# Kernel tuning notes

Measured on AMD Instinct MI355X. Metric: run time of the kernel, lower is better.

## Reference

```python
import jax, jax.numpy as jnp
import numpy as np

B, T, C, H = 8, 1024, 128, 8
BLOCK = 1024  # block_size; wpe has BLOCK+1 rows, last is padding (zeros)
E = C // H


def layer_norm(x, g, b, eps=1e-5):
    mu = jnp.mean(x, axis=-1, keepdims=True)
    var = jnp.var(x, axis=-1, keepdims=True)
    return (x - mu) * jax.lax.rsqrt(var + eps) * g + b


def setup_inputs() -> dict:
    key = jax.random.key(0)
    ks = jax.random.split(key, 7)
    x = jax.random.normal(ks[0], (B, T, C), dtype=jnp.float32)
    Wq = jax.random.normal(ks[1], (C, C), dtype=jnp.float32) * 0.02
    Wk = jax.random.normal(ks[2], (C, C), dtype=jnp.float32) * 0.02
    Wv = jax.random.normal(ks[3], (C, C), dtype=jnp.float32) * 0.02
    Wp = jax.random.normal(ks[4], (C, C), dtype=jnp.float32) * 0.02
    wpe = jax.random.normal(ks[5], (BLOCK + 1, C), dtype=jnp.float32) * 0.02
    wpe = wpe.at[BLOCK].set(0.0)  # padding_idx row is zero
    ln_g = jnp.ones((C,), dtype=jnp.float32)
    ln_b = jnp.zeros((C,), dtype=jnp.float32)
    return {"x": x, "Wq": Wq, "Wk": Wk, "Wv": Wv, "Wp": Wp,
            "wpe": wpe, "ln_g": ln_g, "ln_b": ln_b}


def reference(x, Wq, Wk, Wv, Wp, wpe, ln_g, ln_b):
    Bx, Tx, Cx = x.shape
    ln_x = layer_norm(x, ln_g, ln_b)
    # project and split heads: [B, H, T, E]
    q = (ln_x @ Wq).reshape(Bx, Tx, H, E).transpose(0, 2, 1, 3)
    k = (ln_x @ Wk).reshape(Bx, Tx, H, E).transpose(0, 2, 1, 3)
    v = (ln_x @ Wv).reshape(Bx, Tx, H, E).transpose(0, 2, 1, 3)
    # relative position indices: i-j, negatives -> padding row BLOCK
    i = jnp.arange(Tx)[:, None]
    j = jnp.arange(Tx)[None, :]
    rel_idx = jnp.where(i - j < 0, BLOCK, i - j)  # [T, T]
    rel = wpe[rel_idx].reshape(Tx, Tx, H, E)      # [T, T, H, E]
    scale = 1.0 / np.sqrt(E).astype(np.float32)
    scores = (jnp.einsum('bhte,bhse->bhts', q, k)
              + jnp.einsum('tshe,bhte->bhts', rel, q)) * scale
    causal = (j <= i)  # [T, T]
    scores = jnp.where(causal[None, None, :, :], scores, jnp.float32(-jnp.inf))
    attn = jax.nn.softmax(scores, axis=-1)
    y = jnp.einsum('bhts,bhse->bhte', attn, v)    # [B, H, T, E]
    y = y.transpose(0, 2, 1, 3).reshape(Bx, Tx, Cx)
    return y @ Wp + x
```

## Files before the change

### kernel.cpp

```cpp
#include <hip/hip_runtime.h>
#include <hip/hip_bf16.h>

#define B 8
#define T 1024
#define C 128
#define H 8
#define E 16
#define BH (B*H)

typedef __attribute__((ext_vector_type(4)))  short bf16x4;
typedef __attribute__((ext_vector_type(8)))  short bf16x8;
typedef __attribute__((ext_vector_type(16))) float f32x16;

#define QSCALE 0.36067376022224085f

__device__ __forceinline__ unsigned short bfbits(float x) {
    __hip_bfloat16 h = __float2bfloat16(x);
    return __builtin_bit_cast(unsigned short, h);
}
__device__ __forceinline__ unsigned pack2(float a, float b) {
    return (unsigned)bfbits(a) | ((unsigned)bfbits(b) << 16);
}
__device__ __forceinline__ unsigned packtr(float a, float b) {
    return (__builtin_bit_cast(unsigned, a) >> 16) | (__builtin_bit_cast(unsigned, b) & 0xffff0000u);
}

__global__ __launch_bounds__(C) void k_prep(
    const float* __restrict__ wpe,
    const float* __restrict__ Wq, const float* __restrict__ Wk,
    const float* __restrict__ Wv, const float* __restrict__ Wp,
    __hip_bfloat16* __restrict__ Wpb,
    __hip_bfloat16* __restrict__ WT,
    __hip_bfloat16* __restrict__ WpT)
{
    int bid = blockIdx.x, tid = threadIdx.x;
    if (bid < 1025) {
        int h = tid >> 4, e = tid & 15;
        Wpb[((size_t)h * 1025 + bid) * 16 + e] = __float2bfloat16(wpe[(size_t)bid * C + tid]);
    } else {
        int n = bid - 1025;
        if (n < 128)      WT[n * C + tid]          = __float2bfloat16(Wq[tid * C + n] * QSCALE);
        else if (n < 256) WT[n * C + tid]          = __float2bfloat16(Wk[tid * C + (n - 128)]);
        else if (n < 384) WT[n * C + tid]          = __float2bfloat16(Wv[tid * C + (n - 256)]);
        else              WpT[(n - 384) * C + tid] = __float2bfloat16(Wp[tid * C + (n - 384)]);
    }
}

__global__ __launch_bounds__(256) void k_qkv(
    const float* __restrict__ x, const float* __restrict__ g, const float* __restrict__ bb,
    const __hip_bfloat16* __restrict__ WT,
    __hip_bfloat16* __restrict__ Qb, __hip_bfloat16* __restrict__ Kb,
    __hip_bfloat16* __restrict__ VT)
{
    __shared__ ushort lnlds[32 * 132];
    const int tid = threadIdx.x;
    const int mt = blockIdx.x & 255, part = blockIdx.x >> 8;

    {
        const int r = tid >> 3, qq = tid & 7;
        const float* xp = x + ((size_t)mt * 32 + r) * C + qq * 16;
        float4 x0 = ((const float4*)xp)[0];
        float4 x1 = ((const float4*)xp)[1];
        float4 x2 = ((const float4*)xp)[2];
        float4 x3 = ((const float4*)xp)[3];
        float s1v = x0.x + x0.y + x0.z + x0.w + x1.x + x1.y + x1.z + x1.w
                  + x2.x + x2.y + x2.z + x2.w + x3.x + x3.y + x3.z + x3.w;
        float s2v = x0.x*x0.x + x0.y*x0.y + x0.z*x0.z + x0.w*x0.w
                  + x1.x*x1.x + x1.y*x1.y + x1.z*x1.z + x1.w*x1.w
                  + x2.x*x2.x + x2.y*x2.y + x2.z*x2.z + x2.w*x2.w
                  + x3.x*x3.x + x3.y*x3.y + x3.z*x3.z + x3.w*x3.w;
        s1v += __shfl_xor(s1v, 1, 64); s2v += __shfl_xor(s2v, 1, 64);
        s1v += __shfl_xor(s1v, 2, 64); s2v += __shfl_xor(s2v, 2, 64);
        s1v += __shfl_xor(s1v, 4, 64); s2v += __shfl_xor(s2v, 4, 64);
        float mu  = s1v * (1.f / C);
        float var = s2v * (1.f / C) - mu * mu;
        float rs  = rsqrtf(var + 1e-5f);
        const float4* gp = (const float4*)(g  + qq * 16);
        const float4* bp = (const float4*)(bb + qq * 16);
        float4 g0 = gp[0], g1 = gp[1], g2 = gp[2], g3 = gp[3];
        float4 b0 = bp[0], b1 = bp[1], b2 = bp[2], b3 = bp[3];
        #define LNV(xx, gg, bv) (((xx) - mu) * rs * (gg) + (bv))
        uint2* dst = (uint2*)&lnlds[r * 132 + qq * 16];
        dst[0] = make_uint2(pack2(LNV(x0.x,g0.x,b0.x), LNV(x0.y,g0.y,b0.y)),
                            pack2(LNV(x0.z,g0.z,b0.z), LNV(x0.w,g0.w,b0.w)));
        dst[1] = make_uint2(pack2(LNV(x1.x,g1.x,b1.x), LNV(x1.y,g1.y,b1.y)),
                            pack2(LNV(x1.z,g1.z,b1.z), LNV(x1.w,g1.w,b1.w)));
        dst[2] = make_uint2(pack2(LNV(x2.x,g2.x,b2.x), LNV(x2.y,g2.y,b2.y)),
                            pack2(LNV(x2.z,g2.z,b2.z), LNV(x2.w,g2.w,b2.w)));
        dst[3] = make_uint2(pack2(LNV(x3.x,g3.x,b3.x), LNV(x3.y,g3.y,b3.y)),
                            pack2(LNV(x3.z,g3.z,b3.z), LNV(x3.w,g3.w,b3.w)));
        #undef LNV
    }
    __syncthreads();

    const int wv = tid >> 6, lane = tid & 63, c = lane & 31, h5 = lane >> 5;
    const int b = mt >> 5, trow = (mt & 31) * 32;
    const int nt = part * 4 + wv, n0 = nt * 32;

    bf16x8 wf[8], lf[8];
    #pragma unroll
    for (int s = 0; s < 8; ++s)
        wf[s] = *(const bf16x8*)(WT + (size_t)(n0 + c) * C + 16 * s + 8 * h5);
    #pragma unroll
    for (int s = 0; s < 8; ++s) {
        const ushort* lp = &lnlds[c * 132 + 16 * s + 8 * h5];
        bf16x4 lo = *(const bf16x4*)lp;
        bf16x4 hi = *(const bf16x4*)(lp + 4);
        lf[s] = __builtin_shufflevector(lo, hi, 0, 1, 2, 3, 4, 5, 6, 7);
    }
    f32x16 acc;
    #pragma unroll
    for (int r = 0; r < 16; ++r) acc[r] = 0.f;

    if (nt < 8) {
        #pragma unroll
        for (int s = 0; s < 8; ++s)
            acc = __builtin_amdgcn_mfma_f32_32x32x16_bf16(wf[s], lf[s], acc, 0, 0, 0);
        __hip_bfloat16* base = (nt < 4) ? Qb : Kb;
        const int nb = (nt < 4 ? n0 : n0 - 128) + 4 * h5;
        #pragma unroll
        for (int j2 = 0; j2 < 4; ++j2) {
            int n = nb + 8 * j2;
            int h = n >> 4, e = n & 15;
            uint2 w = make_uint2(pack2(acc[4*j2], acc[4*j2+1]),
                                 pack2(acc[4*j2+2], acc[4*j2+3]));
            *(uint2*)(base + ((size_t)(b * H + h) * T + trow + c) * E + e) = w;
        }
    } else {
        #pragma unroll
        for (int s = 0; s < 8; ++s)
            acc = __builtin_amdgcn_mfma_f32_32x32x16_bf16(lf[s], wf[s], acc, 0, 0, 0);
        const int ecol = n0 - 256 + c;
        const int h = ecol >> 4, e = ecol & 15;
        __hip_bfloat16* vbase = VT + ((size_t)(b * H + h) * E + e) * T + trow + 4 * h5;
        #pragma unroll
        for (int j2 = 0; j2 < 4; ++j2) {
            uint2 w = make_uint2(pack2(acc[4*j2], acc[4*j2+1]),
                                 pack2(acc[4*j2+2], acc[4*j2+3]));
            *(uint2*)(vbase + 8 * j2) = w;
        }
    }
}

__global__ __launch_bounds__(256) void k_attn(
    const __hip_bfloat16* __restrict__ Qb, const __hip_bfloat16* __restrict__ Kb,
    const __hip_bfloat16* __restrict__ VT, const __hip_bfloat16* __restrict__ Wpb,
    __hip_bfloat16* __restrict__ yb)
{
    __shared__ __align__(16) float U_all[4][32 * 68];
    __shared__ float mlb[4][2][32];

    const int tid = threadIdx.x, wv = tid >> 6, lane = tid & 63;
    const int h5 = lane >> 5, c = lane & 31;
    const int bh = blockIdx.x & 63;
    const int jq = 31 - (blockIdx.x >> 6);
    const int hh = bh & (H - 1);
    const int t0 = jq << 5;
    float* Uw = U_all[wv];

    const bf16x8 qf = *(const bf16x8*)(Qb + ((size_t)(bh * T + t0 + c) * E + 8 * h5));

    f32x16 Z, O;
    #pragma unroll
    for (int r = 0; r < 16; ++r) { Z[r] = 0.f; O[r] = 0.f; }
    float m = -1e30f, l = 0.f;

    const bool hd   = ((jq & 3) == wv);
    const int nfull = (jq > wv) ? ((jq - wv + 3) >> 2) : 0;
    const int ntl   = nfull + (hd ? 1 : 0);

    const int s0w = 32 * wv;
    const bf16x8* kp  = (const bf16x8*)(Kb  + ((size_t)(bh * T + s0w + c) * E + 8 * h5));
    const bf16x8* wph = (const bf16x8*)(Wpb + ((size_t)(hh * 1025 + t0 - s0w + c) * E + 8 * h5));
    const bf16x8* wl0 = (const bf16x8*)(Wpb + ((size_t)hh * 1025 * E + 8 * h5));
    const ushort* vap = (const ushort*)(VT + ((size_t)(bh * E + c) * T + s0w + 8 * h5));

    for (int k = 0; k < ntl; ++k) {
        const bool diag = hd && (k == ntl - 1);

        const bf16x8 kf  = *kp;
        const bf16x8 wfh = *wph;
        const bf16x8 wfl = diag ? *wl0 : *(const bf16x8*)((const ushort*)wph - 32 * E);

        f32x16 S   = __builtin_amdgcn_mfma_f32_32x32x16_bf16(kf,  qf, Z, 0, 0, 0);
        f32x16 Ulo = __builtin_amdgcn_mfma_f32_32x32x16_bf16(wfl, qf, Z, 0, 0, 0);
        f32x16 Uhi = __builtin_amdgcn_mfma_f32_32x32x16_bf16(wfh, qf, Z, 0, 0, 0);

        float* up = Uw + c * 68 + 4 * h5;
        *(float4*)(up +  0) = make_float4(Ulo[0],  Ulo[1],  Ulo[2],  Ulo[3]);
        *(float4*)(up +  8) = make_float4(Ulo[4],  Ulo[5],  Ulo[6],  Ulo[7]);
        *(float4*)(up + 16) = make_float4(Ulo[8],  Ulo[9],  Ulo[10], Ulo[11]);
        *(float4*)(up + 24) = make_float4(Ulo[12], Ulo[13], Ulo[14], Ulo[15]);
        *(float4*)(up + 32) = make_float4(Uhi[0],  Uhi[1],  Uhi[2],  Uhi[3]);
        *(float4*)(up + 40) = make_float4(Uhi[4],  Uhi[5],  Uhi[6],  Uhi[7]);
        *(float4*)(up + 48) = make_float4(Uhi[8],  Uhi[9],  Uhi[10], Uhi[11]);
        *(float4*)(up + 56) = make_float4(Uhi[12], Uhi[13], Uhi[14], Uhi[15]);

        const float* ur = Uw + c * 69 + 32 - 4 * h5;
        float sc[16];
        float pmax = -1e30f;
        #pragma unroll
        for (int r = 0; r < 16; ++r) {
            sc[r] = S[r] + ur[-((r & 3) + 8 * (r >> 2))];
            pmax = fmaxf(pmax, sc[r]);
        }
        if (diag) {
            pmax = -1e30f;
            #pragma unroll
            for (int r = 0; r < 16; ++r) {
                const int rowm = 4 * h5 + (r & 3) + 8 * (r >> 2);
                sc[r] = (rowm <= c) ? sc[r] : -1e30f;
                pmax = fmaxf(pmax, sc[r]);
            }
        }
        pmax = fmaxf(pmax, __shfl_xor(pmax, 32, 64));

        if (!__all(pmax <= m)) {
            const float mn = fmaxf(m, pmax);
            const float f = __builtin_amdgcn_exp2f(m - mn);
            l *= f;
            #pragma unroll
            for (int r = 0; r < 8; ++r) O[r] *= f;
            m = mn;
        }
        float p[16];
        float ps = 0.f;
        #pragma unroll
        for (int r = 0; r < 16; ++r) { p[r] = __builtin_amdgcn_exp2f(sc[r] - m); ps += p[r]; }
        ps += __shfl_xor(ps, 32, 64);
        l += ps;

        unsigned w0 = packtr(p[0],  p[1]),  w1 = packtr(p[2],  p[3]);
        unsigned w2 = packtr(p[4],  p[5]),  w3 = packtr(p[6],  p[7]);
        unsigned w4 = packtr(p[8],  p[9]),  w5 = packtr(p[10], p[11]);
        unsigned w6 = packtr(p[12], p[13]), w7 = packtr(p[14], p[15]);
        unsigned r1 = __shfl_xor(h5 ? w0 : w2, 32, 64);
        unsigned r2 = __shfl_xor(h5 ? w1 : w3, 32, 64);
        unsigned r3 = __shfl_xor(h5 ? w4 : w6, 32, 64);
        unsigned r4 = __shfl_xor(h5 ? w5 : w7, 32, 64);
        uint4 f1 = h5 ? make_uint4(r1, r2, w2, w3) : make_uint4(w0, w1, r1, r2);
        uint4 f2 = h5 ? make_uint4(r3, r4, w6, w7) : make_uint4(w4, w5, r3, r4);
        bf16x8 pb1 = __builtin_bit_cast(bf16x8, f1);
        bf16x8 pb2 = __builtin_bit_cast(bf16x8, f2);

        const bf16x8 va = *(const bf16x8*)vap;
        const bf16x8 vb = *(const bf16x8*)(vap + 16);
        O = __builtin_amdgcn_mfma_f32_32x32x16_bf16(va, pb1, O, 0, 0, 0);
        O = __builtin_amdgcn_mfma_f32_32x32x16_bf16(vb, pb2, O, 0, 0, 0);

        kp  = (const bf16x8*)((const ushort*)kp + 128 * E);
        wph = (const bf16x8*)((const ushort*)wph - 128 * E);
        vap += 128;
    }

    __syncthreads();
    float* Of = &U_all[0][0];
    if (h5 == 0) { mlb[wv][0][c] = m; mlb[wv][1][c] = l; }
    float* ob = Of + (wv * 32 + c) * 16;
    *(float4*)(ob + 4 * h5)     = make_float4(O[0], O[1], O[2], O[3]);
    *(float4*)(ob + 4 * h5 + 8) = make_float4(O[4], O[5], O[6], O[7]);
    __syncthreads();
    if (wv == 0) {
        float mx = -1e30f;
        #pragma unroll
        for (int w = 0; w < 4; ++w) mx = fmaxf(mx, mlb[w][0][c]);
        float lt = 0.f;
        float a0=0, a1=0, a2=0, a3=0, b0=0, b1=0, b2=0, b3=0;
        #pragma unroll
        for (int w = 0; w < 4; ++w) {
            float fw = __builtin_amdgcn_exp2f(mlb[w][0][c] - mx);
            lt += mlb[w][1][c] * fw;
            const float* op = Of + (w * 32 + c) * 16;
            float4 o1 = *(const float4*)(op + 4 * h5);
            float4 o2 = *(const float4*)(op + 4 * h5 + 8);
            a0 += o1.x * fw; a1 += o1.y * fw; a2 += o1.z * fw; a3 += o1.w * fw;
            b0 += o2.x * fw; b1 += o2.y * fw; b2 += o2.z * fw; b3 += o2.w * fw;
        }
        float inv = 1.f / lt;
        __hip_bfloat16* yp = yb + ((size_t)((bh >> 3) * T + t0 + c)) * C + (bh & 7) * E + 4 * h5;
        *(uint2*)yp       = make_uint2(pack2(a0 * inv, a1 * inv), pack2(a2 * inv, a3 * inv));
        *(uint2*)(yp + 8) = make_uint2(pack2(b0 * inv, b1 * inv), pack2(b2 * inv, b3 * inv));
    }
}

__global__ __launch_bounds__(256) void k_proj(
    const __hip_bfloat16* __restrict__ yb, const __hip_bfloat16* __restrict__ WpT,
    const float* __restrict__ x, float* __restrict__ out)
{
    __shared__ ushort ylds[32 * 132];
    const int tid = threadIdx.x;
    const size_t row0 = (size_t)blockIdx.x * 32;

    #pragma unroll
    for (int ch = 0; ch < 2; ++ch) {
        int idx = tid + ch * 256;
        int r = idx >> 4, c8 = (idx & 15) * 8;
        const ushort* src = (const ushort*)yb + (row0 + r) * C + c8;
        uint4 a = *(const uint4*)src;
        *(uint2*)&ylds[r * 132 + c8]     = make_uint2(a.x, a.y);
        *(uint2*)&ylds[r * 132 + c8 + 4] = make_uint2(a.z, a.w);
    }
    __syncthreads();

    const int wv = tid >> 6, lane = tid & 63, c = lane & 31, h5 = lane >> 5;
    const int n0 = wv * 32;
    bf16x8 wf[8], yf[8];
    #pragma unroll
    for (int s = 0; s < 8; ++s)
        wf[s] = *(const bf16x8*)(WpT + (size_t)(n0 + c) * C + 16 * s + 8 * h5);
    #pragma unroll
    for (int s = 0; s < 8; ++s) {
        const ushort* lp = &ylds[c * 132 + 16 * s + 8 * h5];
        bf16x4 lo = *(const bf16x4*)lp;
        bf16x4 hi = *(const bf16x4*)(lp + 4);
        yf[s] = __builtin_shufflevector(lo, hi, 0, 1, 2, 3, 4, 5, 6, 7);
    }
    f32x16 acc;
    #pragma unroll
    for (int r = 0; r < 16; ++r) acc[r] = 0.f;
    #pragma unroll
    for (int s = 0; s < 8; ++s)
        acc = __builtin_amdgcn_mfma_f32_32x32x16_bf16(wf[s], yf[s], acc, 0, 0, 0);

    const size_t rb = (row0 + c) * C;
    #pragma unroll
    for (int j2 = 0; j2 < 4; ++j2) {
        int n = n0 + 4 * h5 + 8 * j2;
        float4 xr = *(const float4*)(x + rb + n);
        float4 o  = make_float4(acc[4*j2] + xr.x, acc[4*j2+1] + xr.y,
                                acc[4*j2+2] + xr.z, acc[4*j2+3] + xr.w);
        *(float4*)(out + rb + n) = o;
    }
}

extern "C" void kernel_launch(void* const* d_in, const int* in_sizes, int n_in,
                              void* d_out, int out_size, void* d_ws, size_t ws_size,
                              hipStream_t stream) {
    const float* x   = (const float*)d_in[0];
    const float* Wq  = (const float*)d_in[1];
    const float* Wk  = (const float*)d_in[2];
    const float* Wv  = (const float*)d_in[3];
    const float* Wp  = (const float*)d_in[4];
    const float* wpe = (const float*)d_in[5];
    const float* g   = (const float*)d_in[6];
    const float* bb  = (const float*)d_in[7];
    float* out = (float*)d_out;

    ushort* w = (ushort*)d_ws;
    __hip_bfloat16* Qb  = (__hip_bfloat16*)(w);
    __hip_bfloat16* Kb  = (__hip_bfloat16*)(w + 1048576);
    __hip_bfloat16* VT  = (__hip_bfloat16*)(w + 2097152);
    __hip_bfloat16* Wpb = (__hip_bfloat16*)(w + 3162112);
    __hip_bfloat16* WT  = (__hip_bfloat16*)(w + 3293312);
    __hip_bfloat16* WpT = (__hip_bfloat16*)(w + 3342464);
    __hip_bfloat16* yb  = (__hip_bfloat16*)(w + 3358848);

    k_prep <<<1025 + 512, C,   0, stream>>>(wpe, Wq, Wk, Wv, Wp, Wpb, WT, WpT);
    k_qkv  <<<768,        256, 0, stream>>>(x, g, bb, WT, Qb, Kb, VT);
    k_attn <<<2048,       256, 0, stream>>>(Qb, Kb, VT, Wpb, yb);
    k_proj <<<256,        256, 0, stream>>>(yb, WpT, x, out);
}
```

Before: 43.39 us.

## Fold softmax row-sum into PV MFMA via ones row in V, prefetch K/Wpe

Extends the transposed V buffer with a 17th row of bf16 ones per head so the P·V MFMA produces the softmax denominator in O[8]. This drops the per-iteration sum of p and its cross-lane shuffle. It also software-pipelines the next tile's K and positional-embedding loads, issues the V loads earlier, and rebalances the max reduction into a tree. The cost is a larger VT buffer, an extra prep block group, and a denominator accumulated from bf16-rounded p rather than fp32 values.

```diff
diff --git a/kernel.cpp b/kernel.cpp
--- a/kernel.cpp
+++ b/kernel.cpp
@@ -7,6 +7,7 @@
 #define H 8
 #define E 16
 #define BH (B*H)
+#define VSTR 17
 
 typedef __attribute__((ext_vector_type(4)))  short bf16x4;
 typedef __attribute__((ext_vector_type(8)))  short bf16x8;
@@ -31,18 +32,25 @@
     const float* __restrict__ Wv, const float* __restrict__ Wp,
     __hip_bfloat16* __restrict__ Wpb,
     __hip_bfloat16* __restrict__ WT,
-    __hip_bfloat16* __restrict__ WpT)
+    __hip_bfloat16* __restrict__ WpT,
+    ushort* __restrict__ VT)
 {
     int bid = blockIdx.x, tid = threadIdx.x;
     if (bid < 1025) {
         int h = tid >> 4, e = tid & 15;
         Wpb[((size_t)h * 1025 + bid) * 16 + e] = __float2bfloat16(wpe[(size_t)bid * C + tid]);
-    } else {
+    } else if (bid < 1537) {
         int n = bid - 1025;
         if (n < 128)      WT[n * C + tid]          = __float2bfloat16(Wq[tid * C + n] * QSCALE);
         else if (n < 256) WT[n * C + tid]          = __float2bfloat16(Wk[tid * C + (n - 128)]);
         else if (n < 384) WT[n * C + tid]          = __float2bfloat16(Wv[tid * C + (n - 256)]);
         else              WpT[(n - 384) * C + tid] = __float2bfloat16(Wp[tid * C + (n - 384)]);
+    } else {
+        int bh = bid - 1537;
+        ushort* row = VT + ((size_t)bh * VSTR + 16) * T + tid * 8;
+        uint2 ones = make_uint2(0x3F803F80u, 0x3F803F80u);
+        *(uint2*)(row)     = ones;
+        *(uint2*)(row + 4) = ones;
     }
 }
 
@@ -132,7 +140,7 @@
             acc = __builtin_amdgcn_mfma_f32_32x32x16_bf16(lf[s], wf[s], acc, 0, 0, 0);
         const int ecol = n0 - 256 + c;
         const int h = ecol >> 4, e = ecol & 15;
-        __hip_bfloat16* vbase = VT + ((size_t)(b * H + h) * E + e) * T + trow + 4 * h5;
+        __hip_bfloat16* vbase = VT + ((size_t)(b * H + h) * VSTR + e) * T + trow + 4 * h5;
         #pragma unroll
         for (int j2 = 0; j2 < 4; ++j2) {
             uint2 w = make_uint2(pack2(acc[4*j2], acc[4*j2+1]),
@@ -163,7 +171,7 @@
     f32x16 Z, O;
     #pragma unroll
     for (int r = 0; r < 16; ++r) { Z[r] = 0.f; O[r] = 0.f; }
-    float m = -1e30f, l = 0.f;
+    float m = -1e30f;
 
     const bool hd   = ((jq & 3) == wv);
     const int nfull = (jq > wv) ? ((jq - wv + 3) >> 2) : 0;
@@ -173,14 +181,17 @@
     const bf16x8* kp  = (const bf16x8*)(Kb  + ((size_t)(bh * T + s0w + c) * E + 8 * h5));
     const bf16x8* wph = (const bf16x8*)(Wpb + ((size_t)(hh * 1025 + t0 - s0w + c) * E + 8 * h5));
     const bf16x8* wl0 = (const bf16x8*)(Wpb + ((size_t)hh * 1025 * E + 8 * h5));
-    const ushort* vap = (const ushort*)(VT + ((size_t)(bh * E + c) * T + s0w + 8 * h5));
+    const ushort* vap = (const ushort*)(VT + ((size_t)(bh * VSTR + c) * T + s0w + 8 * h5));
+
+    bf16x8 kf  = *kp;
+    bf16x8 wfh = *wph;
+    bf16x8 wfl = (hd && ntl == 1) ? *wl0 : *(const bf16x8*)((const ushort*)wph - 32 * E);
 
     for (int k = 0; k < ntl; ++k) {
         const bool diag = hd && (k == ntl - 1);
 
-        const bf16x8 kf  = *kp;
-        const bf16x8 wfh = *wph;
-        const bf16x8 wfl = diag ? *wl0 : *(const bf16x8*)((const ushort*)wph - 32 * E);
+        const bf16x8 va = *(const bf16x8*)vap;
+        const bf16x8 vb = *(const bf16x8*)(vap + 16);
 
         f32x16 S   = __builtin_amdgcn_mfma_f32_32x32x16_bf16(kf,  qf, Z, 0, 0, 0);
         f32x16 Ulo = __builtin_amdgcn_mfma_f32_32x32x16_bf16(wfl, qf, Z, 0, 0, 0);
@@ -196,39 +207,45 @@
         *(float4*)(up + 48) = make_float4(Uhi[8],  Uhi[9],  Uhi[10], Uhi[11]);
         *(float4*)(up + 56) = make_float4(Uhi[12], Uhi[13], Uhi[14], Uhi[15]);
 
+        kp  = (const bf16x8*)((const ushort*)kp + 128 * E);
+        wph = (const bf16x8*)((const ushort*)wph - 128 * E);
+        vap += 128;
+        const bool diag_next = hd && (k + 1 == ntl - 1);
+        const bf16x8* wlp = diag_next ? wl0 : (const bf16x8*)((const ushort*)wph - 32 * E);
+        bf16x8 nkf  = *kp;
+        bf16x8 nwfh = *wph;
+        bf16x8 nwfl = *wlp;
+
         const float* ur = Uw + c * 69 + 32 - 4 * h5;
         float sc[16];
-        float pmax = -1e30f;
-        #pragma unroll
-        for (int r = 0; r < 16; ++r) {
+        #pragma unroll
+        for (int r = 0; r < 16; ++r)
             sc[r] = S[r] + ur[-((r & 3) + 8 * (r >> 2))];
-            pmax = fmaxf(pmax, sc[r]);
-        }
         if (diag) {
-            pmax = -1e30f;
             #pragma unroll
             for (int r = 0; r < 16; ++r) {
                 const int rowm = 4 * h5 + (r & 3) + 8 * (r >> 2);
                 sc[r] = (rowm <= c) ? sc[r] : -1e30f;
-                pmax = fmaxf(pmax, sc[r]);
             }
         }
+        float a0 = fmaxf(fmaxf(sc[0],  sc[1]),  sc[2]);
+        float a1 = fmaxf(fmaxf(sc[3],  sc[4]),  sc[5]);
+        float a2 = fmaxf(fmaxf(sc[6],  sc[7]),  sc[8]);
+        float a3 = fmaxf(fmaxf(sc[9],  sc[10]), sc[11]);
+        float a4 = fmaxf(fmaxf(sc[12], sc[13]), sc[14]);
+        float pmax = fmaxf(fmaxf(fmaxf(a0, a1), sc[15]), fmaxf(fmaxf(a2, a3), a4));
         pmax = fmaxf(pmax, __shfl_xor(pmax, 32, 64));
 
         if (!__all(pmax <= m)) {
             const float mn = fmaxf(m, pmax);
             const float f = __builtin_amdgcn_exp2f(m - mn);
-            l *= f;
             #pragma unroll
-            for (int r = 0; r < 8; ++r) O[r] *= f;
+            for (int r = 0; r < 9; ++r) O[r] *= f;
             m = mn;
         }
         float p[16];
-        float ps = 0.f;
-        #pragma unroll
-        for (int r = 0; r < 16; ++r) { p[r] = __builtin_amdgcn_exp2f(sc[r] - m); ps += p[r]; }
-        ps += __shfl_xor(ps, 32, 64);
-        l += ps;
+        #pragma unroll
+        for (int r = 0; r < 16; ++r) p[r] = __builtin_amdgcn_exp2f(sc[r] - m);
 
         unsigned w0 = packtr(p[0],  p[1]),  w1 = packtr(p[2],  p[3]);
         unsigned w2 = packtr(p[4],  p[5]),  w3 = packtr(p[6],  p[7]);
@@ -243,19 +260,15 @@
         bf16x8 pb1 = __builtin_bit_cast(bf16x8, f1);
         bf16x8 pb2 = __builtin_bit_cast(bf16x8, f2);
 
-        const bf16x8 va = *(const bf16x8*)vap;
-        const bf16x8 vb = *(const bf16x8*)(vap + 16);
         O = __builtin_amdgcn_mfma_f32_32x32x16_bf16(va, pb1, O, 0, 0, 0);
         O = __builtin_amdgcn_mfma_f32_32x32x16_bf16(vb, pb2, O, 0, 0, 0);
 
-        kp  = (const bf16x8*)((const ushort*)kp + 128 * E);
-        wph = (const bf16x8*)((const ushort*)wph - 128 * E);
-        vap += 128;
+        kf = nkf; wfh = nwfh; wfl = nwfl;
     }
 
     __syncthreads();
     float* Of = &U_all[0][0];
-    if (h5 == 0) { mlb[wv][0][c] = m; mlb[wv][1][c] = l; }
+    if (h5 == 0) { mlb[wv][0][c] = m; mlb[wv][1][c] = O[8]; }
     float* ob = Of + (wv * 32 + c) * 16;
     *(float4*)(ob + 4 * h5)     = make_float4(O[0], O[1], O[2], O[3]);
     *(float4*)(ob + 4 * h5 + 8) = make_float4(O[4], O[5], O[6], O[7]);
@@ -350,13 +363,13 @@
     __hip_bfloat16* Qb  = (__hip_bfloat16*)(w);
     __hip_bfloat16* Kb  = (__hip_bfloat16*)(w + 1048576);
     __hip_bfloat16* VT  = (__hip_bfloat16*)(w + 2097152);
-    __hip_bfloat16* Wpb = (__hip_bfloat16*)(w + 3162112);
-    __hip_bfloat16* WT  = (__hip_bfloat16*)(w + 3293312);
-    __hip_bfloat16* WpT = (__hip_bfloat16*)(w + 3342464);
-    __hip_bfloat16* yb  = (__hip_bfloat16*)(w + 3358848);
-
-    k_prep <<<1025 + 512, C,   0, stream>>>(wpe, Wq, Wk, Wv, Wp, Wpb, WT, WpT);
-    k_qkv  <<<768,        256, 0, stream>>>(x, g, bb, WT, Qb, Kb, VT);
-    k_attn <<<2048,       256, 0, stream>>>(Qb, Kb, VT, Wpb, yb);
-    k_proj <<<256,        256, 0, stream>>>(yb, WpT, x, out);
-}
+    __hip_bfloat16* Wpb = (__hip_bfloat16*)(w + 3244032);
+    __hip_bfloat16* WT  = (__hip_bfloat16*)(w + 3375232);
+    __hip_bfloat16* WpT = (__hip_bfloat16*)(w + 3424384);
+    __hip_bfloat16* yb  = (__hip_bfloat16*)(w + 3440768);
+
+    k_prep <<<1025 + 512 + 64, C, 0, stream>>>(wpe, Wq, Wk, Wv, Wp, Wpb, WT, WpT, (ushort*)VT);
+    k_qkv  <<<768,  256, 0, stream>>>(x, g, bb, WT, Qb, Kb, VT);
+    k_attn <<<2048, 256, 0, stream>>>(Qb, Kb, VT, Wpb, yb);
+    k_proj <<<256,  256, 0, stream>>>(yb, WpT, x, out);
+}
```

Result: faster. 41.94 us (-3.4%).
